# Optimization experiments

Hardware: AMD Instinct MI355X
Metric: run time of the kernel (lower is better)

## Reference

```python
import jax, jax.numpy as jnp
import numpy as np

B, S0, DE, DT = 32, 255, 768, 256
D = DE + DT          # graph RNN input size
H = 512              # hidden_graph == hidden_edge (required by h_prev[0] = graph_state)
T = 256              # tag_representation_dim
M = 25


def _rnn_layer(x, Wih, Whh, bih, bhh):
    """Vanilla tanh RNN layer, batch_first. x: [B,S,Din] -> [B,S,H]."""
    xW = jnp.einsum('bsd,hd->bsh', x, Wih) + bih  # big GEMM hoisted out of scan
    h0 = jnp.zeros((x.shape[0], Whh.shape[0]), x.dtype)

    def step(h, xw):
        h = jnp.tanh(xw + h @ Whh.T + bhh)
        return h, h

    _, ys = jax.lax.scan(step, h0, jnp.swapaxes(xW, 0, 1))
    return jnp.swapaxes(ys, 0, 1)


def setup_inputs() -> dict:
    key = jax.random.key(0)
    ks = iter(jax.random.split(key, 40))

    def rn(shape, s=1.0):
        return jax.random.normal(next(ks), shape, jnp.float32) * s

    w = 0.04  # ~ uniform(-1/sqrt(H), 1/sqrt(H)) scale of torch RNN init
    return {
        'input': rn((B, S0, DE)),
        'tag_embeddings': rn((B, S0, DT)),
        'mask': jnp.ones((B, S0), jnp.int32),
        'sentinel': rn((D,)),
        'g0_Wih': rn((H, D), w), 'g0_Whh': rn((H, H), w), 'g0_bih': rn((H,), w), 'g0_bhh': rn((H,), w),
        'g1_Wih': rn((H, H), w), 'g1_Whh': rn((H, H), w), 'g1_bih': rn((H,), w), 'g1_bhh': rn((H,), w),
        'e0_Wih': rn((H, 1), w), 'e0_Whh': rn((H, H), w), 'e0_bih': rn((H,), w), 'e0_bhh': rn((H,), w),
        'e1_Wih': rn((H, H), w), 'e1_Whh': rn((H, H), w), 'e1_bih': rn((H,), w), 'e1_bhh': rn((H,), w),
        'cls_W': rn((1, H), w), 'cls_b': rn((1,), w),
        'ht_W': rn((T, H), w), 'ht_b': rn((T,), w),
        'dt_W': rn((T, H), w), 'dt_b': rn((T,), w),
    }


def reference(input, tag_embeddings, mask, sentinel,
              g0_Wih, g0_Whh, g0_bih, g0_bhh,
              g1_Wih, g1_Whh, g1_bih, g1_bhh,
              e0_Wih, e0_Whh, e0_bih, e0_bhh,
              e1_Wih, e1_Whh, e1_bih, e1_bhh,
              cls_W, cls_b, ht_W, ht_b, dt_W, dt_b):
    Bq = input.shape[0]
    x = jnp.concatenate([input, tag_embeddings], axis=-1)              # [B,S0,D]
    sent = jnp.broadcast_to(sentinel[None, None, :], (Bq, 1, x.shape[-1]))
    x = jnp.concatenate([sent, x], axis=1)                             # [B,S,D]
    S = x.shape[1]
    m = jnp.concatenate([jnp.ones((Bq, 1), mask.dtype), mask], axis=1)  # sentinel mask

    # --- graph RNN (2-layer tanh RNN); zero padded outputs == pad_packed_sequence ---
    y = _rnn_layer(x, g0_Wih, g0_Whh, g0_bih, g0_bhh)
    y = _rnn_layer(y, g1_Wih, g1_Whh, g1_bih, g1_bhh)
    graph_state = y * m[..., None].astype(y.dtype)                     # [B,S,H]

    N = Bq * S
    gs = graph_state.reshape(N, -1)        # layer-0 initial hidden
    x0 = jnp.ones((N, 1), graph_state.dtype)
    h1_0 = jnp.zeros_like(gs)              # layer-1 initial hidden

    def step(carry, _):
        xe, h0, h1 = carry
        h0 = jnp.tanh(xe @ e0_Wih.T + e0_bih + h0 @ e0_Whh.T + e0_bhh)
        h1 = jnp.tanh(h0 @ e1_Wih.T + e1_bih + h1 @ e1_Whh.T + e1_bhh)
        pred = h1 @ cls_W.T + cls_b        # [N,1]
        return (pred, h0, h1), pred

    _, preds = jax.lax.scan(step, (x0, gs, h1_0), None, length=M)      # [M,N,1]
    A = jnp.concatenate([x0[:, None, :], jnp.swapaxes(preds, 0, 1)], axis=1)[..., 0]  # [N,M+1]

    # --- reshape_adj: banded GraphRNN predictions -> square adjacency logits ---
    A3 = A.reshape(Bq, S, M + 1)
    i = jnp.arange(S)[:, None]
    j = jnp.arange(S)[None, :]
    k = i - j                                # offset of node j behind node i
    valid = (k >= 0) & (k <= M)
    rows = jnp.broadcast_to(i, (S, S))
    arc = A3[:, rows, jnp.clip(k, 0, M)]     # [B,S,S]
    arc_logits = jnp.where(valid[None], arc, jnp.zeros((), arc.dtype))

    # --- tag heads (dropout is identity at eval) ---
    head_tag = jax.nn.elu(graph_state @ ht_W.T + ht_b)
    dep_tag = jax.nn.elu(graph_state @ dt_W.T + dt_b)
    return arc_logits, head_tag, dep_tag
```

## Files before the change

### kernel.cpp

```cpp
#include <hip/hip_runtime.h>
#include <math.h>

typedef unsigned int u32;
typedef unsigned short u16;
typedef unsigned long long u64;
typedef __attribute__((ext_vector_type(8))) short short8;
typedef __attribute__((ext_vector_type(4))) float f32x4;

__device__ inline float bf2f(u16 v) { return __uint_as_float(((u32)v) << 16); }
__device__ inline u16 f2bf(float f) {
  u32 u = __float_as_uint(f);
  return (u16)((u + 0x7fffu + ((u >> 16) & 1u)) >> 16);
}
__device__ inline float fast_tanh(float x) {
  x = fminf(9.0f, fmaxf(-9.0f, x));
  float e = __builtin_amdgcn_exp2f(x * 2.8853900817779268f);
  return (e - 1.0f) * __builtin_amdgcn_rcpf(e + 1.0f);
}
__device__ inline void gload16(const void* g, void* l) {
  __builtin_amdgcn_global_load_lds((const __attribute__((address_space(1))) u32*)g,
                                   (__attribute__((address_space(3))) u32*)l, 16, 0, 0);
}

__device__ inline void tile_map(int blk, int& m0, int& n0) {
  n0 = (blk >> 6) << 7;
  m0 = (blk & 63) << 7;
}

__global__ void k_prep1(u16* __restrict__ xhi, u16* __restrict__ xlo,
                        const float* __restrict__ inp, const float* __restrict__ tag,
                        const float* __restrict__ sent,
                        u16* __restrict__ w0hi, u16* __restrict__ w0lo,
                        const float* __restrict__ g0wih,
                        float* __restrict__ wt0, const float* __restrict__ g0whh,
                        float* __restrict__ wt1, const float* __restrict__ g1whh,
                        u16* __restrict__ g1hi, u16* __restrict__ g1lo,
                        const float* __restrict__ g1wih) {
  int blk = blockIdx.x, t = threadIdx.x;
  if (blk < 32768) {
    int gid = blk * 256 + t;
    int row = gid >> 10, c = gid & 1023;
    int b = row >> 8, s = row & 255;
    float v;
    if (s == 0) v = sent[c];
    else if (c < 768) v = inp[(size_t)(b * 255 + s - 1) * 768 + c];
    else v = tag[(size_t)(b * 255 + s - 1) * 256 + (c - 768)];
    u16 h = f2bf(v);
    xhi[gid] = h;
    xlo[gid] = f2bf(v - bf2f(h));
  } else if (blk < 34816) {
    int i = (blk - 32768) * 256 + t;
    float v = g0wih[i];
    u16 h = f2bf(v);
    w0hi[i] = h;
    w0lo[i] = f2bf(v - bf2f(h));
  } else if (blk < 35840) {
    int i = (blk - 34816) * 256 + t;
    int k = i & 511, tt = i >> 9;
    wt0[(size_t)k * 512 + tt] = g0whh[(size_t)tt * 512 + k];
  } else if (blk < 36864) {
    int i = (blk - 35840) * 256 + t;
    int k = i & 511, tt = i >> 9;
    wt1[(size_t)k * 512 + tt] = g1whh[(size_t)tt * 512 + k];
  } else {
    int i = (blk - 36864) * 256 + t;
    float v = g1wih[i];
    u16 h = f2bf(v);
    g1hi[i] = h;
    g1lo[i] = f2bf(v - bf2f(h));
  }
}

__global__ void k_prep2(u64* __restrict__ hbuf,
                        u16* __restrict__ w0b, const float* __restrict__ e0whh,
                        u16* __restrict__ w1b, const float* __restrict__ e1wih,
                        u16* __restrict__ w2b, const float* __restrict__ e1whh,
                        u16* __restrict__ w3b, const float* __restrict__ htw,
                        u16* __restrict__ w4b, const float* __restrict__ dtw,
                        float* __restrict__ abuf, const float* __restrict__ clsb) {
  int blk = blockIdx.x, t = threadIdx.x;
  if (blk < 128) {
    int i = blk * 256 + t;
    int pos = i & 1023;
    hbuf[i] = (pos < 512) ? (1ull << 32) : 0ull;
  } else if (blk < 1152) {
    int i = (blk - 128) * 256 + t;  w0b[i] = f2bf(e0whh[i]);
  } else if (blk < 2176) {
    int i = (blk - 1152) * 256 + t; w1b[i] = f2bf(e1wih[i]);
  } else if (blk < 3200) {
    int i = (blk - 2176) * 256 + t; w2b[i] = f2bf(e1whh[i]);
  } else if (blk < 3712) {
    int i = (blk - 3200) * 256 + t; w3b[i] = f2bf(htw[i]);
  } else if (blk < 4224) {
    int i = (blk - 3712) * 256 + t; w4b[i] = f2bf(dtw[i]);
  } else {
    int i = (blk - 4224) * 256 + t;
    if (i < 212992) abuf[i] = ((i % 26) == 0) ? 1.0f : clsb[0];
  }
}

__global__ void k_prep3(u64* __restrict__ hbuf, uint4* __restrict__ s1) {
  int blk = blockIdx.x, t = threadIdx.x;
  if (blk < 128) {
    int i = blk * 256 + t;
    int pos = i & 1023;
    hbuf[i] = (pos < 512) ? (1ull << 32) : 0ull;
  } else {
    s1[(size_t)(blk - 128) * 256 + t] = uint4{0u, 0u, 0u, 0u};
  }
}

__global__ __launch_bounds__(512, 1) void k_gscan_mb(
    const float* __restrict__ XW, const float* __restrict__ WT,
    const int* __restrict__ mask, int layer, u64* hbuf,
    u16* __restrict__ o16a, u16* __restrict__ o16b)
{
  __shared__ float hls[2][528];
  const int blk = blockIdx.x;
  const int b = blk >> 2, q = blk & 3;
  const int tid = threadIdx.x;
  const int lane = tid & 63;
  const int wv = tid >> 6;
  const int colL = wv * 16 + (lane & 15);
  const int p = (lane >> 4) & 3;
  const int c = (q << 7) + colL;
  const bool fin = (p == 0);
  float wreg[128];
#pragma unroll
  for (int i = 0; i < 128; ++i)
    wreg[i] = WT[(size_t)(p * 128 + i) * 512 + c];
  u64* hb = hbuf + b * 1024;

  for (int s = 0; s < 256; ++s) {
    float xwv = 0.f;
    size_t off = 0;
    if (fin) {
      off = (size_t)(b * 256 + s) * 512 + c;
      xwv = XW[off];
    }
    const u32 want = (u32)(s + 1);
    u64 v;
    do {
      v = __hip_atomic_load(&hb[(s & 1) * 512 + tid], __ATOMIC_RELAXED,
                            __HIP_MEMORY_SCOPE_AGENT);
    } while ((u32)(v >> 32) < want);
    hls[s & 1][(tid >> 7) * 132 + (tid & 127)] = __uint_as_float((u32)v);
    __syncthreads();
    const float* hk = &hls[s & 1][p * 132];
    float a0 = 0.f, a1 = 0.f, a2 = 0.f, a3 = 0.f;
#pragma unroll
    for (int i = 0; i < 128; i += 4) {
      a0 = fmaf(wreg[i],     hk[i],     a0);
      a1 = fmaf(wreg[i + 1], hk[i + 1], a1);
      a2 = fmaf(wreg[i + 2], hk[i + 2], a2);
      a3 = fmaf(wreg[i + 3], hk[i + 3], a3);
    }
    float r = (a0 + a1) + (a2 + a3);
    r += __shfl_xor(r, 16);
    r += __shfl_xor(r, 32);
    if (fin) {
      float h = tanhf(r + xwv);
      u64 pk = ((u64)(u32)(s + 2) << 32) | (u64)__float_as_uint(h);
      __hip_atomic_store(&hb[((s + 1) & 1) * 512 + c], pk,
                         __ATOMIC_RELAXED, __HIP_MEMORY_SCOPE_AGENT);
      if (layer) {
        float mv = (s == 0) ? 1.f : (float)mask[b * 255 + s - 1];
        o16a[off] = f2bf(h * mv);
      } else {
        u16 hi = f2bf(h);
        o16a[off] = hi;
        o16b[off] = f2bf(h - bf2f(hi));
      }
    }
  }
}

template<int KD>
__global__ __launch_bounds__(256, 2) void gemm_s(
    const u16* __restrict__ Ahi, const u16* __restrict__ Alo,
    const u16* __restrict__ Whi, const u16* __restrict__ Wlo,
    const float* __restrict__ b1, const float* __restrict__ b2,
    float* __restrict__ outf)
{
  __shared__ __attribute__((aligned(16))) u16 Ah[128 * 64];
  __shared__ __attribute__((aligned(16))) u16 Al[128 * 64];
  __shared__ __attribute__((aligned(16))) u16 Wh[128 * 64];
  __shared__ __attribute__((aligned(16))) u16 Wl[128 * 64];
  const int tid = threadIdx.x;
  const int lane = tid & 63, wid = tid >> 6;
  const int wr = wid >> 1, wc = wid & 1;
  int m0, n0;
  tile_map(blockIdx.x, m0, n0);
  const int rsub = lane >> 3;
  const int swz = (((lane & 7) ^ rsub) << 3);

  f32x4 zero4 = {0.f, 0.f, 0.f, 0.f};
  f32x4 acc[4][4];
#pragma unroll
  for (int i = 0; i < 4; ++i)
#pragma unroll
    for (int j = 0; j < 4; ++j) acc[i][j] = zero4;

  for (int kt = 0; kt < KD / 64; ++kt) {
    __syncthreads();
#pragma unroll
    for (int cc = 0; cc < 4; ++cc) {
      int row = wid * 32 + cc * 8 + rsub;
      size_t ga = (size_t)(m0 + row) * KD + kt * 64 + swz;
      size_t gw = (size_t)(n0 + row) * KD + kt * 64 + swz;
      gload16(Ahi + ga, &Ah[(wid * 32 + cc * 8) * 64]);
      gload16(Alo + ga, &Al[(wid * 32 + cc * 8) * 64]);
      gload16(Whi + gw, &Wh[(wid * 32 + cc * 8) * 64]);
      gload16(Wlo + gw, &Wl[(wid * 32 + cc * 8) * 64]);
    }
    __syncthreads();
#pragma unroll
    for (int ks = 0; ks < 2; ++ks) {
      short8 ah[4], al[4], wh[4], wl[4];
#pragma unroll
      for (int mm = 0; mm < 4; ++mm) {
        int row = wr * 64 + mm * 16 + (lane & 15);
        int kb = (ks * 64 + ((lane >> 4) << 4)) ^ ((row & 7) << 4);
        ah[mm] = *(const short8*)((const char*)Ah + row * 128 + kb);
        al[mm] = *(const short8*)((const char*)Al + row * 128 + kb);
      }
#pragma unroll
      for (int nn = 0; nn < 4; ++nn) {
        int row = wc * 64 + nn * 16 + (lane & 15);
        int kb = (ks * 64 + ((lane >> 4) << 4)) ^ ((row & 7) << 4);
        wh[nn] = *(const short8*)((const char*)Wh + row * 128 + kb);
        wl[nn] = *(const short8*)((const char*)Wl + row * 128 + kb);
      }
#pragma unroll
      for (int mm = 0; mm < 4; ++mm)
#pragma unroll
        for (int nn = 0; nn < 4; ++nn) {
          acc[mm][nn] = __builtin_amdgcn_mfma_f32_16x16x32_bf16(ah[mm], wh[nn], acc[mm][nn], 0, 0, 0);
          acc[mm][nn] = __builtin_amdgcn_mfma_f32_16x16x32_bf16(ah[mm], wl[nn], acc[mm][nn], 0, 0, 0);
          acc[mm][nn] = __builtin_amdgcn_mfma_f32_16x16x32_bf16(al[mm], wh[nn], acc[mm][nn], 0, 0, 0);
        }
    }
  }

  float bcol[4];
#pragma unroll
  for (int nn = 0; nn < 4; ++nn) {
    int col = n0 + wc * 64 + nn * 16 + (lane & 15);
    bcol[nn] = b1[col] + b2[col];
  }
#pragma unroll
  for (int mm = 0; mm < 4; ++mm)
#pragma unroll
    for (int r = 0; r < 4; ++r) {
      int grow = m0 + wr * 64 + mm * 16 + ((lane >> 4) << 2) + r;
#pragma unroll
      for (int nn = 0; nn < 4; ++nn) {
        int col = n0 + wc * 64 + nn * 16 + (lane & 15);
        outf[(size_t)grow * 512 + col] = acc[mm][nn][r] + bcol[nn];
      }
    }
}

template<int MODE, int KD>
__global__ __launch_bounds__(256, 2) void gemm_k(
    const u16* __restrict__ Ag, const u16* __restrict__ Ag2,
    const u16* __restrict__ Wg, const u16* __restrict__ W2g,
    const float* __restrict__ b1, const float* __restrict__ b2,
    u16* __restrict__ outb, float* __restrict__ outh, float* __restrict__ outd,
    float* __restrict__ abuf, const float* __restrict__ vecw, int estep)
{
  __shared__ __attribute__((aligned(16))) u16 As[128 * 64];
  __shared__ __attribute__((aligned(16))) u16 Ws[128 * 64];
  __shared__ float xes[128];
  const int tid = threadIdx.x;
  const int lane = tid & 63, wid = tid >> 6;
  const int wr = wid >> 1, wc = wid & 1;
  int m0, n0;
  tile_map(blockIdx.x, m0, n0);
  const int rsub = lane >> 3;
  const int swz = (((lane & 7) ^ rsub) << 3);

  if constexpr (MODE == 2) {
    if (tid < 128) xes[tid] = abuf[(size_t)(m0 + tid) * 26 + estep];
  }

  f32x4 zero4 = {0.f, 0.f, 0.f, 0.f};
  f32x4 acc[4][4];
#pragma unroll
  for (int i = 0; i < 4; ++i)
#pragma unroll
    for (int j = 0; j < 4; ++j) acc[i][j] = zero4;

  for (int kt = 0; kt < KD / 64; ++kt) {
    const u16* Asrc; int ka;
    if (kt < 8) { Asrc = Ag;  ka = kt; }
    else        { Asrc = Ag2; ka = kt - 8; }
    const u16* Wsrc; int kw, rowoff;
    if constexpr (MODE == 1) {
      if (n0 >= 256) { Wsrc = W2g; rowoff = n0 - 256; }
      else           { Wsrc = Wg;  rowoff = n0; }
      kw = kt;
    } else {
      if (kt < 8) { Wsrc = Wg;  kw = kt; }
      else        { Wsrc = W2g; kw = kt - 8; }
      rowoff = n0;
    }
    __syncthreads();
#pragma unroll
    for (int cc = 0; cc < 4; ++cc) {
      int row = wid * 32 + cc * 8 + rsub;
      gload16(Asrc + (size_t)(m0 + row) * 512 + ka * 64 + swz, &As[(wid * 32 + cc * 8) * 64]);
      gload16(Wsrc + (size_t)(rowoff + row) * 512 + kw * 64 + swz, &Ws[(wid * 32 + cc * 8) * 64]);
    }
    __syncthreads();
#pragma unroll
    for (int ks = 0; ks < 2; ++ks) {
      short8 af[4], wf[4];
#pragma unroll
      for (int mm = 0; mm < 4; ++mm) {
        int row = wr * 64 + mm * 16 + (lane & 15);
        int kb = (ks * 64 + ((lane >> 4) << 4)) ^ ((row & 7) << 4);
        af[mm] = *(const short8*)((const char*)As + row * 128 + kb);
      }
#pragma unroll
      for (int nn = 0; nn < 4; ++nn) {
        int row = wc * 64 + nn * 16 + (lane & 15);
        int kb = (ks * 64 + ((lane >> 4) << 4)) ^ ((row & 7) << 4);
        wf[nn] = *(const short8*)((const char*)Ws + row * 128 + kb);
      }
#pragma unroll
      for (int mm = 0; mm < 4; ++mm)
#pragma unroll
        for (int nn = 0; nn < 4; ++nn)
          acc[mm][nn] = __builtin_amdgcn_mfma_f32_16x16x32_bf16(af[mm], wf[nn], acc[mm][nn], 0, 0, 0);
    }
  }

  float bcol[4], vcol[4];
#pragma unroll
  for (int nn = 0; nn < 4; ++nn) {
    int col = n0 + wc * 64 + nn * 16 + (lane & 15);
    if constexpr (MODE == 1) bcol[nn] = (col < 256) ? b1[col] : b2[col - 256];
    else                     bcol[nn] = b1[col] + b2[col];
    vcol[nn] = 0.0f;
    if constexpr (MODE == 2 || MODE == 3) vcol[nn] = vecw[col];
  }
  float pp[4][4];
#pragma unroll
  for (int i = 0; i < 4; ++i)
#pragma unroll
    for (int j = 0; j < 4; ++j) pp[i][j] = 0.0f;

#pragma unroll
  for (int mm = 0; mm < 4; ++mm) {
#pragma unroll
    for (int r = 0; r < 4; ++r) {
      int lrow = wr * 64 + mm * 16 + ((lane >> 4) << 2) + r;
      int grow = m0 + lrow;
#pragma unroll
      for (int nn = 0; nn < 4; ++nn) {
        int col = n0 + wc * 64 + nn * 16 + (lane & 15);
        float v = acc[mm][nn][r] + bcol[nn];
        if constexpr (MODE == 1) {
          float e = v > 0.f ? v : (expf(v) - 1.f);
          if (col < 256) outh[(size_t)grow * 256 + col] = e;
          else           outd[(size_t)grow * 256 + (col - 256)] = e;
        } else if constexpr (MODE == 2) {
          v += xes[lrow] * vcol[nn];
          outb[(size_t)grow * 512 + col] = f2bf(fast_tanh(v));
        } else {
          float h = fast_tanh(v);
          outb[(size_t)grow * 512 + col] = f2bf(h);
          pp[mm][r] += h * vcol[nn];
        }
      }
    }
  }
  if constexpr (MODE == 3) {
#pragma unroll
    for (int mm = 0; mm < 4; ++mm)
#pragma unroll
      for (int r = 0; r < 4; ++r) {
        float p = pp[mm][r];
        p += __shfl_xor(p, 1); p += __shfl_xor(p, 2);
        p += __shfl_xor(p, 4); p += __shfl_xor(p, 8);
        if ((lane & 15) == 0) {
          int grow = m0 + wr * 64 + mm * 16 + ((lane >> 4) << 2) + r;
          atomicAdd(&abuf[(size_t)grow * 26 + estep + 1], p);
        }
      }
  }
}

__global__ void k_arc(float* __restrict__ outp, const float* __restrict__ abuf) {
  int idx = blockIdx.x * 256 + threadIdx.x;
  int j = idx & 255, i = (idx >> 8) & 255, b = idx >> 16;
  int k = i - j;
  outp[idx] = (k >= 0 && k <= 25) ? abuf[(size_t)(b * 256 + i) * 26 + k] : 0.0f;
}
__global__ void k_diag(float* __restrict__ outp, float code, int n) {
  int idx = blockIdx.x * 256 + threadIdx.x;
  if (idx < n) outp[idx] = (idx == 0) ? code : 0.0f;
}

extern "C" void kernel_launch(void* const* d_in, const int* in_sizes, int n_in,
                              void* d_out, int out_size, void* d_ws, size_t ws_size,
                              hipStream_t stream) {
  static const int SZ[26] = {6266880, 2088960, 8160, 1024, 524288, 262144, 512, 512,
                             262144, 262144, 512, 512, 512, 262144, 512, 512,
                             262144, 262144, 512, 512, 512, 1, 131072, 256, 131072, 256};
  float diag_code = 0.0f;
  if (n_in != 26) diag_code = 4096.0f + (float)n_in;
  else {
    for (int j = 0; j < 26; ++j)
      if (in_sizes[j] != SZ[j]) { diag_code = 2048.0f + (float)j; break; }
  }
  const size_t NEED = (size_t)(32u << 20);
  if (ws_size < NEED && diag_code == 0.0f) diag_code = 8192.0f;
  if (diag_code != 0.0f) {
    k_diag<<<(out_size + 255) / 256, 256, 0, stream>>>((float*)d_out, diag_code, out_size);
    return;
  }

  const float* inp  = (const float*)d_in[0];
  const float* tag  = (const float*)d_in[1];
  const int*   mask = (const int*)d_in[2];
  const float* sent = (const float*)d_in[3];
  const float* g0_Wih = (const float*)d_in[4];
  const float* g0_Whh = (const float*)d_in[5];
  const float* g0_bih = (const float*)d_in[6];
  const float* g0_bhh = (const float*)d_in[7];
  const float* g1_Wih = (const float*)d_in[8];
  const float* g1_Whh = (const float*)d_in[9];
  const float* g1_bih = (const float*)d_in[10];
  const float* g1_bhh = (const float*)d_in[11];
  const float* e0_Wih = (const float*)d_in[12];
  const float* e0_Whh = (const float*)d_in[13];
  const float* e0_bih = (const float*)d_in[14];
  const float* e0_bhh = (const float*)d_in[15];
  const float* e1_Wih = (const float*)d_in[16];
  const float* e1_Whh = (const float*)d_in[17];
  const float* e1_bih = (const float*)d_in[18];
  const float* e1_bhh = (const float*)d_in[19];
  const float* cls_W  = (const float*)d_in[20];
  const float* cls_b  = (const float*)d_in[21];
  const float* ht_W   = (const float*)d_in[22];
  const float* ht_b   = (const float*)d_in[23];
  const float* dt_W   = (const float*)d_in[24];
  const float* dt_b   = (const float*)d_in[25];

  float* out = (float*)d_out;
  char*  ob  = (char*)d_out;
  char*  ws  = (char*)d_ws;

  u16*  W0hi = (u16*)(ob);
  u16*  W0lo = (u16*)(ob + (1u << 20));
  float* XW0 = (float*)(ob + (2u << 20));
  float* WT0 = (float*)(ob + (18u << 20));
  float* WT1 = (float*)(ob + (19u << 20));
  u16*  G1hi = (u16*)(ob + (20u << 20));
  u16*  G1lo = (u16*)(ob + (20u << 20) + (512u << 10));
  u16*  Xhi  = (u16*)(ws);
  u16*  Xlo  = (u16*)(ws + (16u << 20));
  u16*  Y0hi = (u16*)(ws);
  u16*  Y0lo = (u16*)(ws + (8u << 20));
  u16*  S0   = Y0hi;
  u16*  S1   = Y0lo;
  u16*  S2   = (u16*)(ws + (16u << 20));
  float* ABUF = (float*)(ws + (24u << 20));
  u16*  W0b  = (u16*)(ws + (25u << 20));
  u16*  W1b  = (u16*)(ws + (25u << 20) + (512u << 10));
  u16*  W2b  = (u16*)(ws + (26u << 20));
  u16*  W3b  = (u16*)(ws + (26u << 20) + (512u << 10));
  u16*  W4b  = (u16*)(ws + (26u << 20) + (768u << 10));
  u64*  HBUF = (u64*)(ws + (28u << 20));

  k_prep1<<<37888, 256, 0, stream>>>(Xhi, Xlo, inp, tag, sent,
                                     W0hi, W0lo, g0_Wih, WT0, g0_Whh, WT1, g1_Whh,
                                     G1hi, G1lo, g1_Wih);
  gemm_s<1024><<<256, 256, 0, stream>>>(Xhi, Xlo, W0hi, W0lo, g0_bih, g0_bhh, XW0);
  k_prep2<<<5056, 256, 0, stream>>>(HBUF, W0b, e0_Whh, W1b, e1_Wih, W2b, e1_Whh,
                                    W3b, ht_W, W4b, dt_W, ABUF, cls_b);
  k_gscan_mb<<<128, 512, 0, stream>>>(XW0, WT0, mask, 0, HBUF, Y0hi, Y0lo);
  gemm_s<512><<<256, 256, 0, stream>>>(Y0hi, Y0lo, G1hi, G1lo, g1_bih, g1_bhh, XW0);
  k_prep3<<<2176, 256, 0, stream>>>(HBUF, (uint4*)S1);
  k_gscan_mb<<<128, 512, 0, stream>>>(XW0, WT1, mask, 1, HBUF, S0, nullptr);
  gemm_k<1, 512><<<256, 256, 0, stream>>>(S0, nullptr, W3b, W4b, ht_b, dt_b,
                                          nullptr, out + 2097152, out + 4194304,
                                          nullptr, nullptr, 0);
  u16* r0 = S0; u16* r1 = S1; u16* r2 = S2;
  for (int st = 0; st < 25; ++st) {
    gemm_k<2, 512><<<256, 256, 0, stream>>>(r0, nullptr, W0b, nullptr, e0_bih, e0_bhh,
                                            r2, nullptr, nullptr, ABUF, e0_Wih, st);
    gemm_k<3, 1024><<<256, 256, 0, stream>>>(r2, r1, W1b, W2b, e1_bih, e1_bhh,
                                             r0, nullptr, nullptr, ABUF, cls_W, st);
    u16* t0 = r2; u16* t1 = r0; u16* t2 = r1;
    r0 = t0; r1 = t1; r2 = t2;
  }
  k_arc<<<8192, 256, 0, stream>>>(out, ABUF);
}
```

Baseline: 1.668 ms.

## Fuse 25-step edge RNN into one persistent kernel with LDS-resident hidden state

```diff
diff --git a/kernel.cpp b/kernel.cpp
--- a/kernel.cpp
+++ b/kernel.cpp
@@ -99,15 +99,10 @@
   }
 }
 
-__global__ void k_prep3(u64* __restrict__ hbuf, uint4* __restrict__ s1) {
-  int blk = blockIdx.x, t = threadIdx.x;
-  if (blk < 128) {
-    int i = blk * 256 + t;
-    int pos = i & 1023;
-    hbuf[i] = (pos < 512) ? (1ull << 32) : 0ull;
-  } else {
-    s1[(size_t)(blk - 128) * 256 + t] = uint4{0u, 0u, 0u, 0u};
-  }
+__global__ void k_prep3(u64* __restrict__ hbuf) {
+  int i = blockIdx.x * 256 + threadIdx.x;
+  int pos = i & 1023;
+  hbuf[i] = (pos < 512) ? (1ull << 32) : 0ull;
 }
 
 __global__ __launch_bounds__(512, 1) void k_gscan_mb(
@@ -172,6 +167,202 @@
         o16b[off] = f2bf(h - bf2f(hi));
       }
     }
+  }
+}
+
+__global__ __launch_bounds__(256, 1) void k_edge_fused(
+    const u16* __restrict__ S0,
+    const u16* __restrict__ W0b, const u16* __restrict__ W1b, const u16* __restrict__ W2b,
+    const float* __restrict__ e0Wih,
+    const float* __restrict__ e0bi, const float* __restrict__ e0bh,
+    const float* __restrict__ e1bi, const float* __restrict__ e1bh,
+    const float* __restrict__ clsW, const float* __restrict__ clsb,
+    float* __restrict__ abuf)
+{
+  __shared__ __attribute__((aligned(16))) u16 h0b[32 * 512];
+  __shared__ __attribute__((aligned(16))) u16 h1b[32 * 512];
+  __shared__ __attribute__((aligned(16))) u16 Wst[4][128 * 64];
+  __shared__ float xesh[32];
+  __shared__ float red[4][32];
+  const int tid = threadIdx.x;
+  const int lane = tid & 63, w = tid >> 6;
+  const int lrow = lane & 15, lk = lane >> 4;
+  const int r0 = blockIdx.x * 32;
+  const int c0 = w * 128;
+  const int rsub = lane >> 3;
+  const int swz = (((lane & 7) ^ rsub) << 3);
+
+#pragma unroll
+  for (int i = 0; i < 8; ++i) {
+    int gidx = tid + i * 256;
+    int row = gidx >> 6, g = gidx & 63;
+    short8 v = *(const short8*)(S0 + (size_t)(r0 + row) * 512 + g * 8);
+    int sg = g ^ (row & 7);
+    *(short8*)(&h0b[row * 512 + sg * 8]) = v;
+    short8 z = {0, 0, 0, 0, 0, 0, 0, 0};
+    *(short8*)(&h1b[row * 512 + sg * 8]) = z;
+  }
+  if (tid < 32) xesh[tid] = 1.0f;
+  float b0c[8], b1c[8], wihc[8], cwc[8];
+#pragma unroll
+  for (int nn = 0; nn < 8; ++nn) {
+    int col = c0 + nn * 16 + lrow;
+    b0c[nn] = e0bi[col] + e0bh[col];
+    b1c[nn] = e1bi[col] + e1bh[col];
+    wihc[nn] = e0Wih[col];
+    cwc[nn] = clsW[col];
+  }
+  const float cb = clsb[0];
+  __syncthreads();
+
+  f32x4 zero4 = {0.f, 0.f, 0.f, 0.f};
+
+  for (int st = 0; st < 25; ++st) {
+    f32x4 acc[2][8];
+#pragma unroll
+    for (int mt = 0; mt < 2; ++mt)
+#pragma unroll
+      for (int nn = 0; nn < 8; ++nn) acc[mt][nn] = zero4;
+#pragma unroll 1
+    for (int kt = 0; kt < 8; ++kt) {
+      asm volatile("s_waitcnt lgkmcnt(0)" ::: "memory");
+#pragma unroll
+      for (int cc = 0; cc < 16; ++cc) {
+        int row = cc * 8 + rsub;
+        gload16(W0b + (size_t)(c0 + row) * 512 + kt * 64 + swz, &Wst[w][cc * 512]);
+      }
+      asm volatile("s_waitcnt vmcnt(0)" ::: "memory");
+      __builtin_amdgcn_sched_barrier(0);
+#pragma unroll
+      for (int ks = 0; ks < 2; ++ks) {
+        short8 af[2];
+#pragma unroll
+        for (int mt = 0; mt < 2; ++mt) {
+          int arow = mt * 16 + lrow;
+          int g = (kt * 8 + ks * 4 + lk) ^ (arow & 7);
+          af[mt] = *(const short8*)(&h0b[arow * 512 + g * 8]);
+        }
+#pragma unroll
+        for (int nn = 0; nn < 8; ++nn) {
+          int brow = nn * 16 + lrow;
+          int kb = (ks * 64 + (lk << 4)) ^ ((brow & 7) << 4);
+          short8 bf = *(const short8*)((const char*)&Wst[w][0] + brow * 128 + kb);
+#pragma unroll
+          for (int mt = 0; mt < 2; ++mt)
+            acc[mt][nn] = __builtin_amdgcn_mfma_f32_16x16x32_bf16(af[mt], bf, acc[mt][nn], 0, 0, 0);
+        }
+      }
+    }
+#pragma unroll
+    for (int mt = 0; mt < 2; ++mt)
+#pragma unroll
+      for (int nn = 0; nn < 8; ++nn)
+#pragma unroll
+        for (int ri = 0; ri < 4; ++ri) {
+          int row = mt * 16 + lk * 4 + ri;
+          acc[mt][nn][ri] = fast_tanh(acc[mt][nn][ri] + b0c[nn] + xesh[row] * wihc[nn]);
+        }
+    __syncthreads();
+#pragma unroll
+    for (int mt = 0; mt < 2; ++mt)
+#pragma unroll
+      for (int nn = 0; nn < 8; ++nn)
+#pragma unroll
+        for (int ri = 0; ri < 4; ++ri) {
+          int row = mt * 16 + lk * 4 + ri;
+          int col = c0 + nn * 16 + lrow;
+          int sg = (col >> 3) ^ (row & 7);
+          h0b[row * 512 + sg * 8 + (col & 7)] = f2bf(acc[mt][nn][ri]);
+        }
+    __syncthreads();
+
+#pragma unroll
+    for (int mt = 0; mt < 2; ++mt)
+#pragma unroll
+      for (int nn = 0; nn < 8; ++nn) acc[mt][nn] = zero4;
+#pragma unroll 1
+    for (int kt = 0; kt < 16; ++kt) {
+      const u16* Wsrc = (kt < 8) ? W1b : W2b;
+      const u16* Asrc = (kt < 8) ? h0b : h1b;
+      int kl = (kt < 8) ? kt : (kt - 8);
+      asm volatile("s_waitcnt lgkmcnt(0)" ::: "memory");
+#pragma unroll
+      for (int cc = 0; cc < 16; ++cc) {
+        int row = cc * 8 + rsub;
+        gload16(Wsrc + (size_t)(c0 + row) * 512 + kl * 64 + swz, &Wst[w][cc * 512]);
+      }
+      asm volatile("s_waitcnt vmcnt(0)" ::: "memory");
+      __builtin_amdgcn_sched_barrier(0);
+#pragma unroll
+      for (int ks = 0; ks < 2; ++ks) {
+        short8 af[2];
+#pragma unroll
+        for (int mt = 0; mt < 2; ++mt) {
+          int arow = mt * 16 + lrow;
+          int g = (kl * 8 + ks * 4 + lk) ^ (arow & 7);
+          af[mt] = *(const short8*)(&Asrc[arow * 512 + g * 8]);
+        }
+#pragma unroll
+        for (int nn = 0; nn < 8; ++nn) {
+          int brow = nn * 16 + lrow;
+          int kb = (ks * 64 + (lk << 4)) ^ ((brow & 7) << 4);
+          short8 bf = *(const short8*)((const char*)&Wst[w][0] + brow * 128 + kb);
+#pragma unroll
+          for (int mt = 0; mt < 2; ++mt)
+            acc[mt][nn] = __builtin_amdgcn_mfma_f32_16x16x32_bf16(af[mt], bf, acc[mt][nn], 0, 0, 0);
+        }
+      }
+    }
+    float pp[2][4];
+#pragma unroll
+    for (int mt = 0; mt < 2; ++mt)
+#pragma unroll
+      for (int ri = 0; ri < 4; ++ri) pp[mt][ri] = 0.f;
+#pragma unroll
+    for (int mt = 0; mt < 2; ++mt)
+#pragma unroll
+      for (int nn = 0; nn < 8; ++nn)
+#pragma unroll
+        for (int ri = 0; ri < 4; ++ri) {
+          float h = fast_tanh(acc[mt][nn][ri] + b1c[nn]);
+          acc[mt][nn][ri] = h;
+          pp[mt][ri] += h * cwc[nn];
+        }
+#pragma unroll
+    for (int mt = 0; mt < 2; ++mt)
+#pragma unroll
+      for (int ri = 0; ri < 4; ++ri) {
+        float p = pp[mt][ri];
+        p += __shfl_xor(p, 1); p += __shfl_xor(p, 2);
+        p += __shfl_xor(p, 4); p += __shfl_xor(p, 8);
+        pp[mt][ri] = p;
+      }
+    __syncthreads();
+#pragma unroll
+    for (int mt = 0; mt < 2; ++mt)
+#pragma unroll
+      for (int nn = 0; nn < 8; ++nn)
+#pragma unroll
+        for (int ri = 0; ri < 4; ++ri) {
+          int row = mt * 16 + lk * 4 + ri;
+          int col = c0 + nn * 16 + lrow;
+          int sg = (col >> 3) ^ (row & 7);
+          h1b[row * 512 + sg * 8 + (col & 7)] = f2bf(acc[mt][nn][ri]);
+        }
+    if (lrow == 0) {
+#pragma unroll
+      for (int mt = 0; mt < 2; ++mt)
+#pragma unroll
+        for (int ri = 0; ri < 4; ++ri)
+          red[w][mt * 16 + lk * 4 + ri] = pp[mt][ri];
+    }
+    __syncthreads();
+    if (tid < 32) {
+      float pred = cb + ((red[0][tid] + red[1][tid]) + (red[2][tid] + red[3][tid]));
+      xesh[tid] = pred;
+      abuf[(size_t)(r0 + tid) * 26 + st + 1] = pred;
+    }
+    __syncthreads();
   }
 }
 
@@ -271,7 +462,6 @@
 {
   __shared__ __attribute__((aligned(16))) u16 As[128 * 64];
   __shared__ __attribute__((aligned(16))) u16 Ws[128 * 64];
-  __shared__ float xes[128];
   const int tid = threadIdx.x;
   const int lane = tid & 63, wid = tid >> 6;
   const int wr = wid >> 1, wc = wid & 1;
@@ -280,10 +470,6 @@
   const int rsub = lane >> 3;
   const int swz = (((lane & 7) ^ rsub) << 3);
 
-  if constexpr (MODE == 2) {
-    if (tid < 128) xes[tid] = abuf[(size_t)(m0 + tid) * 26 + estep];
-  }
-
   f32x4 zero4 = {0.f, 0.f, 0.f, 0.f};
   f32x4 acc[4][4];
 #pragma unroll
@@ -292,19 +478,11 @@
     for (int j = 0; j < 4; ++j) acc[i][j] = zero4;
 
   for (int kt = 0; kt < KD / 64; ++kt) {
-    const u16* Asrc; int ka;
-    if (kt < 8) { Asrc = Ag;  ka = kt; }
-    else        { Asrc = Ag2; ka = kt - 8; }
+    const u16* Asrc = Ag; int ka = kt;
     const u16* Wsrc; int kw, rowoff;
-    if constexpr (MODE == 1) {
-      if (n0 >= 256) { Wsrc = W2g; rowoff = n0 - 256; }
-      else           { Wsrc = Wg;  rowoff = n0; }
-      kw = kt;
-    } else {
-      if (kt < 8) { Wsrc = Wg;  kw = kt; }
-      else        { Wsrc = W2g; kw = kt - 8; }
-      rowoff = n0;
-    }
+    if (n0 >= 256) { Wsrc = W2g; rowoff = n0 - 256; }
+    else           { Wsrc = Wg;  rowoff = n0; }
+    kw = kt;
     __syncthreads();
 #pragma unroll
     for (int cc = 0; cc < 4; ++cc) {
@@ -336,59 +514,26 @@
     }
   }
 
-  float bcol[4], vcol[4];
+  float bcol[4];
 #pragma unroll
   for (int nn = 0; nn < 4; ++nn) {
     int col = n0 + wc * 64 + nn * 16 + (lane & 15);
-    if constexpr (MODE == 1) bcol[nn] = (col < 256) ? b1[col] : b2[col - 256];
-    else                     bcol[nn] = b1[col] + b2[col];
-    vcol[nn] = 0.0f;
-    if constexpr (MODE == 2 || MODE == 3) vcol[nn] = vecw[col];
-  }
-  float pp[4][4];
-#pragma unroll
-  for (int i = 0; i < 4; ++i)
-#pragma unroll
-    for (int j = 0; j < 4; ++j) pp[i][j] = 0.0f;
-
+    bcol[nn] = (col < 256) ? b1[col] : b2[col - 256];
+  }
 #pragma unroll
   for (int mm = 0; mm < 4; ++mm) {
 #pragma unroll
     for (int r = 0; r < 4; ++r) {
-      int lrow = wr * 64 + mm * 16 + ((lane >> 4) << 2) + r;
-      int grow = m0 + lrow;
+      int grow = m0 + wr * 64 + mm * 16 + ((lane >> 4) << 2) + r;
 #pragma unroll
       for (int nn = 0; nn < 4; ++nn) {
         int col = n0 + wc * 64 + nn * 16 + (lane & 15);
         float v = acc[mm][nn][r] + bcol[nn];
-        if constexpr (MODE == 1) {
-          float e = v > 0.f ? v : (expf(v) - 1.f);
-          if (col < 256) outh[(size_t)grow * 256 + col] = e;
-          else           outd[(size_t)grow * 256 + (col - 256)] = e;
-        } else if constexpr (MODE == 2) {
-          v += xes[lrow] * vcol[nn];
-          outb[(size_t)grow * 512 + col] = f2bf(fast_tanh(v));
-        } else {
-          float h = fast_tanh(v);
-          outb[(size_t)grow * 512 + col] = f2bf(h);
-          pp[mm][r] += h * vcol[nn];
-        }
-      }
-    }
-  }
-  if constexpr (MODE == 3) {
-#pragma unroll
-    for (int mm = 0; mm < 4; ++mm)
-#pragma unroll
-      for (int r = 0; r < 4; ++r) {
-        float p = pp[mm][r];
-        p += __shfl_xor(p, 1); p += __shfl_xor(p, 2);
-        p += __shfl_xor(p, 4); p += __shfl_xor(p, 8);
-        if ((lane & 15) == 0) {
-          int grow = m0 + wr * 64 + mm * 16 + ((lane >> 4) << 2) + r;
-          atomicAdd(&abuf[(size_t)grow * 26 + estep + 1], p);
-        }
-      }
+        float e = v > 0.f ? v : (expf(v) - 1.f);
+        if (col < 256) outh[(size_t)grow * 256 + col] = e;
+        else           outd[(size_t)grow * 256 + (col - 256)] = e;
+      }
+    }
   }
 }
 
@@ -465,8 +610,6 @@
   u16*  Y0hi = (u16*)(ws);
   u16*  Y0lo = (u16*)(ws + (8u << 20));
   u16*  S0   = Y0hi;
-  u16*  S1   = Y0lo;
-  u16*  S2   = (u16*)(ws + (16u << 20));
   float* ABUF = (float*)(ws + (24u << 20));
   u16*  W0b  = (u16*)(ws + (25u << 20));
   u16*  W1b  = (u16*)(ws + (25u << 20) + (512u << 10));
@@ -483,19 +626,13 @@
                                     W3b, ht_W, W4b, dt_W, ABUF, cls_b);
   k_gscan_mb<<<128, 512, 0, stream>>>(XW0, WT0, mask, 0, HBUF, Y0hi, Y0lo);
   gemm_s<512><<<256, 256, 0, stream>>>(Y0hi, Y0lo, G1hi, G1lo, g1_bih, g1_bhh, XW0);
-  k_prep3<<<2176, 256, 0, stream>>>(HBUF, (uint4*)S1);
+  k_prep3<<<128, 256, 0, stream>>>(HBUF);
   k_gscan_mb<<<128, 512, 0, stream>>>(XW0, WT1, mask, 1, HBUF, S0, nullptr);
   gemm_k<1, 512><<<256, 256, 0, stream>>>(S0, nullptr, W3b, W4b, ht_b, dt_b,
                                           nullptr, out + 2097152, out + 4194304,
                                           nullptr, nullptr, 0);
-  u16* r0 = S0; u16* r1 = S1; u16* r2 = S2;
-  for (int st = 0; st < 25; ++st) {
-    gemm_k<2, 512><<<256, 256, 0, stream>>>(r0, nullptr, W0b, nullptr, e0_bih, e0_bhh,
-                                            r2, nullptr, nullptr, ABUF, e0_Wih, st);
-    gemm_k<3, 1024><<<256, 256, 0, stream>>>(r2, r1, W1b, W2b, e1_bih, e1_bhh,
-                                             r0, nullptr, nullptr, ABUF, cls_W, st);
-    u16* t0 = r2; u16* t1 = r0; u16* t2 = r1;
-    r0 = t0; r1 = t1; r2 = t2;
-  }
+  k_edge_fused<<<256, 256, 0, stream>>>(S0, W0b, W1b, W2b, e0_Wih,
+                                        e0_bih, e0_bhh, e1_bih, e1_bhh,
+                                        cls_W, cls_b, ABUF);
   k_arc<<<8192, 256, 0, stream>>>(out, ABUF);
 }
```

After: 1.716 ms. +2.9%, slower.
